# Optimization experiments

Hardware: AMD Instinct MI355X
Metric: run time of the kernel (lower is better)

Reference implementation:

```python
import jax, jax.numpy as jnp
import numpy as np

NFFT = 1024
HOP = 512
N_FREQ = NFFT // 2
B = 16
T = 4096


def _istft_kernels(nfft):
    # Same construction as _get_istft_kernels in the torch source.
    t = np.arange(nfft, dtype=np.float64)[:, None]
    f = np.arange(nfft // 2 + 1, dtype=np.float64)[None, :]
    k = np.exp(1j * (2.0 * np.pi * t * f) / nfft)  # [nfft, nfft/2+1]
    ac_cof = float(np.real(k[0, 0]))  # == 1.0
    k = 2.0 * k[:, 1:]
    k[:, -1] = k[:, -1] / 2.0
    return (np.real(k).astype(np.float32),  # [nfft, n_freq]
            np.imag(k).astype(np.float32),
            ac_cof)


def setup_inputs() -> dict:
    key = jax.random.key(0)
    k1, k2, k3 = jax.random.split(key, 3)
    magn = jax.random.normal(k1, (B, 1, N_FREQ, T), dtype=jnp.float32)
    phase = jax.random.normal(k2, (B, 1, N_FREQ, T), dtype=jnp.float32)
    ac = jax.random.normal(k3, (B, 1, T), dtype=jnp.float32)
    rk, ik, _ = _istft_kernels(NFFT)
    return {
        "magn": magn,
        "phase": phase,
        "ac": ac,
        "real_kernels": jnp.asarray(rk),   # [nfft, n_freq]
        "imag_kernels": jnp.asarray(ik),   # [nfft, n_freq]
    }


def reference(magn, phase, ac, real_kernels, imag_kernels):
    nfft, hop = NFFT, HOP
    ac_cof = 1.0  # real(exp(0)) from kernels[0, 0]
    real_part = jnp.einsum('bft,of->bot', magn[:, 0], real_kernels)   # [B, nfft, T]
    imag_part = jnp.einsum('bft,of->bot', -phase[:, 0], imag_kernels)  # [B, nfft, T]
    frames = (real_part - imag_part + ac_cof * ac) / float(nfft)       # ac [B,1,T] broadcasts
    # conv_transpose2d with identity kernel [nfft,1,1,nfft], stride=hop == overlap-add
    b, _, t = frames.shape
    out_len = (t - 1) * hop + nfft
    idx = jnp.arange(t)[:, None] * hop + jnp.arange(nfft)[None, :]     # [T, nfft]
    sig = jnp.zeros((b, out_len), frames.dtype)
    sig = sig.at[:, idx].add(jnp.swapaxes(frames, 1, 2))               # scatter-add frames
    return sig
```

## Files before the change

### kernel.cpp

```cpp
#include <hip/hip_runtime.h>
#include <hip/hip_bf16.h>

typedef __bf16 bf16;
typedef __bf16 bf16x4 __attribute__((ext_vector_type(4)));
typedef __bf16 bf16x8 __attribute__((ext_vector_type(8)));
typedef float  f32x4  __attribute__((ext_vector_type(4)));

#define T_SZ   4096
#define NFREQ  512
#define HOP    512
#define OUT_LEN 2097664
#define NTT33  33
#define XROWS  4097

#define XW_ELEMS ((size_t)16 * XROWS * 1024)
#define WT_ELEMS ((size_t)512 * 1024)
#define WS_NEED  ((XW_ELEMS + WT_ELEMS) * 2)

__device__ __forceinline__ void gl16(const void* g, void* l) {
    __builtin_amdgcn_global_load_lds(
        (const __attribute__((address_space(1))) void*)g,
        (__attribute__((address_space(3))) void*)l, 16, 0, 0);
}


__global__ __launch_bounds__(256, 4) void cvt_w(const float* __restrict__ rk,
                                                const float* __restrict__ ik,
                                                bf16* __restrict__ Wt) {
    const int j  = blockIdx.x;
    const int k4 = threadIdx.x * 4;
    const float* s = (k4 < NFREQ) ? &rk[j * NFREQ + k4] : &ik[j * NFREQ + k4 - NFREQ];
    f32x4 v = *(const f32x4*)s;
    bf16x4 h;
    h[0] = (bf16)v[0]; h[1] = (bf16)v[1]; h[2] = (bf16)v[2]; h[3] = (bf16)v[3];
    *(bf16x4*)&Wt[((size_t)j << 10) + k4] = h;
}

__global__ __launch_bounds__(256, 4) void cvt_x(const float* __restrict__ magn,
                                                const float* __restrict__ phase,
                                                bf16* __restrict__ Xw) {
    __shared__ float t2[64][133];
    const int tid = threadIdx.x;
    const int bid = blockIdx.x;
    const int kt  = bid & 15;
    const int tt  = (bid >> 4) & 31;
    const int b   = bid >> 9;
    const float* srcb = (kt < 8 ? magn : phase)
                      + ((size_t)b * NFREQ + (kt & 7) * 64) * T_SZ + tt * 128;
    const int fr = tid >> 5;
    const int cc = (tid & 31) * 4;
    #pragma unroll
    for (int p = 0; p < 8; ++p) {
        const int f = fr + 8 * p;
        f32x4 v = *(const f32x4*)&srcb[(size_t)f * T_SZ + cc];
        t2[f][cc + 0] = v[0]; t2[f][cc + 1] = v[1];
        t2[f][cc + 2] = v[2]; t2[f][cc + 3] = v[3];
    }
    if (tid < 64)
        t2[tid][128] = (tt > 0) ? srcb[(size_t)tid * T_SZ - 1] : 0.f;
    __syncthreads();

    const int koff = (tid & 7) * 8;
    bf16* dstb = Xw + (((size_t)b * XROWS + tt * 128) << 10) + kt * 64 + koff;
    #pragma unroll
    for (int q = 0; q < 4; ++q) {
        const int tr  = (tid >> 3) + 32 * q;
        const int im1 = tr ? (tr - 1) : 128;
        bf16x8 o;
        #pragma unroll
        for (int ki = 0; ki < 8; ++ki) {
            const int f = koff + ki;
            const float sgn = (f & 1) ? 1.f : -1.f;
            o[ki] = (bf16)(t2[f][tr] + sgn * t2[f][im1]);
        }
        *(bf16x8*)&dstb[(size_t)tr << 10] = o;
    }
    if (tt == 31 && tid < 8) {
        bf16x8 o;
        #pragma unroll
        for (int ki = 0; ki < 8; ++ki) {
            const int f = tid * 8 + ki;
            const float sgn = (f & 1) ? 1.f : -1.f;
            o[ki] = (bf16)(sgn * t2[f][127]);
        }
        *(bf16x8*)&Xw[(((size_t)b * XROWS + 4096) << 10) + kt * 64 + tid * 8] = o;
    }
}

__global__ __launch_bounds__(512, 4) void istft_gemmY(
    const bf16* __restrict__ Xw, const bf16* __restrict__ Wt,
    const float* __restrict__ acv, float* __restrict__ out)
{
    __shared__ __attribute__((aligned(16))) bf16 As[2][128 * 32];
    __shared__ __attribute__((aligned(16))) bf16 Bs[2][256 * 32];

    const int tid = threadIdx.x;
    const int w   = tid >> 6;
    const int l   = tid & 63;
    const int wr  = w >> 2, wc = w & 3;
    const int c15 = l & 15, c4 = l >> 4;

    const int bid = blockIdx.x;
    const int xcd = bid & 7;
    const int jt  = (bid >> 3) & 3;
    const int pg  = bid >> 5;
    const int pnl = pg * 8 + xcd;
    const int b   = pnl / 17;
    const int tt0 = pnl - b * 17;
    const int j0  = jt * 128;
    const int t0  = tt0 * 256;
    const size_t xb = (size_t)b * XROWS;

    const int ssrc = ((l & 3) ^ ((l >> 2) & 3) ^ ((l >> 4) & 3)) * 8;
    const int srow = 16 * w + (l >> 2);
    const size_t asrc = ((size_t)(j0 + srow)) << 10;
    int tq0 = t0 + srow;        if (tq0 > 4096) tq0 = 4096;
    int tq1 = t0 + 128 + srow;  if (tq1 > 4096) tq1 = 4096;
    const size_t bsrc0 = (xb + tq0) << 10;
    const size_t bsrc1 = (xb + tq1) << 10;

    auto stage = [&](int p, int ks) {
        const int k0 = ks * 32;
        gl16(Wt + asrc + k0 + ssrc, &As[p][(16 * w) * 32]);
        gl16(Xw + bsrc0 + k0 + ssrc, &Bs[p][(16 * w) * 32]);
        gl16(Xw + bsrc1 + k0 + ssrc, &Bs[p][(128 + 16 * w) * 32]);
    };

    f32x4 acc[4][4];
    #pragma unroll
    for (int i = 0; i < 4; ++i)
        #pragma unroll
        for (int j = 0; j < 4; ++j)
            acc[i][j] = (f32x4){0.f, 0.f, 0.f, 0.f};

    bf16x8 a[4], bb[4];
    auto rdFrags = [&](int p) {
        #pragma unroll
        for (int m = 0; m < 4; ++m) {
            const int r = wr * 64 + m * 16 + c15;
            const int s = ((c4 ^ r ^ (r >> 2)) & 3) * 8;
            a[m] = *(const bf16x8*)&As[p][r * 32 + s];
        }
        #pragma unroll
        for (int n = 0; n < 4; ++n) {
            const int r = wc * 64 + n * 16 + c15;
            const int s = ((c4 ^ r ^ (r >> 2)) & 3) * 8;
            bb[n] = *(const bf16x8*)&Bs[p][r * 32 + s];
        }
    };

    stage(0, 0);
    __syncthreads();

    for (int ks = 0; ks < 32; ++ks) {
        const int P = ks & 1;
        if (ks + 1 < 32) stage(P ^ 1, ks + 1);
        rdFrags(P);
        #pragma unroll
        for (int m = 0; m < 4; ++m)
            #pragma unroll
            for (int n = 0; n < 4; ++n)
                acc[m][n] = __builtin_amdgcn_mfma_f32_16x16x32_bf16(
                    a[m], bb[n], acc[m][n], 0, 0, 0);
        __syncthreads();
    }

    const float inv = 1.0f / 1024.0f;
    float* ob = out + (size_t)b * OUT_LEN;
    const float* acb = acv + (size_t)b * T_SZ;
    const int jbase = j0 + wr * 64 + c4 * 4;
    #pragma unroll
    for (int n = 0; n < 4; ++n) {
        const int tt = t0 + wc * 64 + n * 16 + c15;
        if (tt <= 4096) {
            const float acs = (tt < T_SZ ? acb[tt] : 0.f) + (tt ? acb[tt - 1] : 0.f);
            #pragma unroll
            for (int m = 0; m < 4; ++m) {
                f32x4 v;
                #pragma unroll
                for (int rr = 0; rr < 4; ++rr)
                    v[rr] = (acc[m][n][rr] + acs) * inv;
                __builtin_nontemporal_store(v, (f32x4*)&ob[(size_t)tt * HOP + jbase + m * 16]);
            }
        }
    }
}

#define LDBL 40
__global__ __launch_bounds__(256, 2) void istft_fused_legacy(
    const float* __restrict__ magn, const float* __restrict__ phase,
    const float* __restrict__ acv,
    const float* __restrict__ rk,  const float* __restrict__ ik,
    float* __restrict__ out)
{
    __shared__ __attribute__((aligned(16))) bf16 As[2][128 * LDBL];
    __shared__ __attribute__((aligned(16))) bf16 Bs[2][129 * LDBL];
    const int tid = threadIdx.x;
    const int w = tid >> 6, l = tid & 63;
    const int bid = blockIdx.x;
    const int xcd = bid & 7, q = bid >> 3;
    const int jt = q & 7, pgrp = q >> 3;
    const int pnl = pgrp * 8 + xcd;
    const int b = pnl / NTT33, tt0 = pnl - b * NTT33;
    const int j0 = jt * 64, t0 = tt0 * 128;
    const float* xm = magn  + (size_t)b * NFREQ * T_SZ;
    const float* xp = phase + (size_t)b * NFREQ * T_SZ;
    const int jrow = tid >> 3, fc = (tid & 7) * 4;
    const int f0 = (tid >> 5) * 4, tl = tid & 31;
    f32x4 areg[4]; float vreg[4][4]; float rz = 0.f;
    f32x4 acc[8][2];
    #pragma unroll
    for (int i = 0; i < 8; ++i)
        #pragma unroll
        for (int j = 0; j < 2; ++j) acc[i][j] = (f32x4){0.f, 0.f, 0.f, 0.f};
    const int nbase = w * 32;
    auto loadA = [&](int ks) {
        const int k0 = ks * 32;
        const float* wsrc = (k0 < NFREQ) ? (rk + k0) : (ik + (k0 - NFREQ));
        #pragma unroll
        for (int i = 0; i < 4; ++i) {
            const int jr = jrow + 32 * i;
            const int j = (jr < 64) ? (j0 + jr) : (j0 + 448 + jr);
            areg[i] = *(const f32x4*)&wsrc[(size_t)j * NFREQ + fc];
        }
    };
    auto writeA = [&](int p) {
        #pragma unroll
        for (int i = 0; i < 4; ++i) {
            bf16x4 v;
            v[0] = (bf16)areg[i][0]; v[1] = (bf16)areg[i][1];
            v[2] = (bf16)areg[i][2]; v[3] = (bf16)areg[i][3];
            *(bf16x4*)&As[p][(jrow + 32 * i) * LDBL + fc] = v;
        }
    };
    auto loadB = [&](int ks) {
        const int k0 = ks * 32;
        const float* xbp = (k0 < NFREQ) ? (xm + (size_t)k0 * T_SZ)
                                        : (xp + (size_t)(k0 - NFREQ) * T_SZ);
        #pragma unroll
        for (int i = 0; i < 4; ++i) {
            if (t0 + 32 * i + 32 <= T_SZ) {
                #pragma unroll
                for (int fj = 0; fj < 4; ++fj)
                    vreg[fj][i] = xbp[(size_t)(f0 + fj) * T_SZ + t0 + tl + 32 * i];
            } else {
                #pragma unroll
                for (int fj = 0; fj < 4; ++fj) vreg[fj][i] = 0.f;
            }
        }
        if (tid < 32) rz = (t0 >= 1) ? xbp[(size_t)tid * T_SZ + (t0 - 1)] : 0.f;
    };
    auto writeB = [&](int p) {
        #pragma unroll
        for (int i = 0; i < 4; ++i) {
            bf16x4 v;
            v[0] = (bf16)vreg[0][i]; v[1] = (bf16)vreg[1][i];
            v[2] = (bf16)vreg[2][i]; v[3] = (bf16)vreg[3][i];
            *(bf16x4*)&Bs[p][(1 + tl + 32 * i) * LDBL + f0] = v;
        }
        if (tid < 32) Bs[p][tid] = (bf16)rz;
    };
    loadA(0); loadB(0); writeA(0); writeB(0);
    __syncthreads();
    int p = 0;
    for (int ks = 0; ks < 32; ++ks) {
        if (ks + 1 < 32) { loadA(ks + 1); loadB(ks + 1); }
        bf16x8 af[8], blv[2], bhv[2];
        #pragma unroll
        for (int mi = 0; mi < 8; ++mi)
            af[mi] = *(const bf16x8*)&As[p][(mi * 16 + (l & 15)) * LDBL + (l >> 4) * 8];
        #pragma unroll
        for (int ni = 0; ni < 2; ++ni) {
            const int rb = nbase + ni * 16 + (l & 15);
            bhv[ni] = *(const bf16x8*)&Bs[p][rb * LDBL + (l >> 4) * 8];
            blv[ni] = *(const bf16x8*)&Bs[p][(rb + 1) * LDBL + (l >> 4) * 8];
        }
        #pragma unroll
        for (int ni = 0; ni < 2; ++ni)
            #pragma unroll
            for (int mi = 0; mi < 4; ++mi) {
                acc[mi][ni] = __builtin_amdgcn_mfma_f32_16x16x32_bf16(af[mi], blv[ni], acc[mi][ni], 0, 0, 0);
                acc[mi + 4][ni] = __builtin_amdgcn_mfma_f32_16x16x32_bf16(af[mi + 4], bhv[ni], acc[mi + 4][ni], 0, 0, 0);
            }
        if (ks + 1 < 32) { writeA(p ^ 1); writeB(p ^ 1); }
        __syncthreads();
        p ^= 1;
    }
    const float inv = 1.0f / 1024.0f;
    float* ob = out + (size_t)b * OUT_LEN;
    const float* acb = acv + (size_t)b * T_SZ;
    #pragma unroll
    for (int ni = 0; ni < 2; ++ni) {
        const int tt = t0 + nbase + ni * 16 + (l & 15);
        if (tt <= T_SZ) {
            float acs = 0.f;
            if (tt < T_SZ) acs += acb[tt];
            if (tt >= 1)   acs += acb[tt - 1];
            #pragma unroll
            for (int mi = 0; mi < 4; ++mi) {
                const int jl = j0 + mi * 16 + (l >> 4) * 4;
                f32x4 v;
                #pragma unroll
                for (int rr = 0; rr < 4; ++rr)
                    v[rr] = (acc[mi][ni][rr] + acc[mi + 4][ni][rr] + acs) * inv;
                __builtin_nontemporal_store(v, (f32x4*)&ob[(size_t)tt * HOP + jl]);
            }
        }
    }
}

extern "C" void kernel_launch(void* const* d_in, const int* in_sizes, int n_in,
                              void* d_out, int out_size, void* d_ws, size_t ws_size,
                              hipStream_t stream) {
    const float* magn  = (const float*)d_in[0];
    const float* phase = (const float*)d_in[1];
    const float* ac    = (const float*)d_in[2];
    const float* rk    = (const float*)d_in[3];
    const float* ik    = (const float*)d_in[4];
    float* out = (float*)d_out;

    if (ws_size >= WS_NEED) {
        bf16* Xw = (bf16*)d_ws;
        bf16* Wt = Xw + XW_ELEMS;
        cvt_w<<<512, 256, 0, stream>>>(rk, ik, Wt);
        cvt_x<<<8192, 256, 0, stream>>>(magn, phase, Xw);
        istft_gemmY<<<1088, 512, 0, stream>>>(Xw, Wt, ac, out);
    } else {
        istft_fused_legacy<<<528 * 8, 256, 0, stream>>>(magn, phase, ac, rk, ik, out);
    }
}
```

Measured before the change: 179.3 us.

## Split GEMM into even 128x128 tiles and move the ragged last row to a tail kernel

The main GEMM changes from 512-thread blocks with 128x256 tiles (17 t-tiles per batch, the last one ragged) to 256-thread blocks with 128x128 tiles over exactly 4096 rows, so the grid is uniform and the bounds checks go away. The single leftover output row (t=4096) is computed by a separate small GEMV kernel with 16 blocks. This is meant to remove load imbalance and tail waste from the padded tile. In exchange each tile reuses less data and the extra launch adds overhead.

After: 205.3 us. 14.5% more time.

```diff
diff --git a/kernel.cpp b/kernel.cpp
--- a/kernel.cpp
+++ b/kernel.cpp
@@ -87,17 +87,17 @@
     }
 }
 
-__global__ __launch_bounds__(512, 4) void istft_gemmY(
+__global__ __launch_bounds__(256, 4) void istft_gemmY2(
     const bf16* __restrict__ Xw, const bf16* __restrict__ Wt,
     const float* __restrict__ acv, float* __restrict__ out)
 {
     __shared__ __attribute__((aligned(16))) bf16 As[2][128 * 32];
-    __shared__ __attribute__((aligned(16))) bf16 Bs[2][256 * 32];
+    __shared__ __attribute__((aligned(16))) bf16 Bs[2][128 * 32];
 
     const int tid = threadIdx.x;
     const int w   = tid >> 6;
     const int l   = tid & 63;
-    const int wr  = w >> 2, wc = w & 3;
+    const int wr  = w >> 1, wc = w & 1;
     const int c15 = l & 15, c4 = l >> 4;
 
     const int bid = blockIdx.x;
@@ -105,25 +105,26 @@
     const int jt  = (bid >> 3) & 3;
     const int pg  = bid >> 5;
     const int pnl = pg * 8 + xcd;
-    const int b   = pnl / 17;
-    const int tt0 = pnl - b * 17;
+    const int b   = pnl >> 5;
+    const int tt0 = pnl & 31;
     const int j0  = jt * 128;
-    const int t0  = tt0 * 256;
+    const int t0  = tt0 * 128;
     const size_t xb = (size_t)b * XROWS;
 
     const int ssrc = ((l & 3) ^ ((l >> 2) & 3) ^ ((l >> 4) & 3)) * 8;
     const int srow = 16 * w + (l >> 2);
-    const size_t asrc = ((size_t)(j0 + srow)) << 10;
-    int tq0 = t0 + srow;        if (tq0 > 4096) tq0 = 4096;
-    int tq1 = t0 + 128 + srow;  if (tq1 > 4096) tq1 = 4096;
-    const size_t bsrc0 = (xb + tq0) << 10;
-    const size_t bsrc1 = (xb + tq1) << 10;
+
+    const size_t asrc0 = ((size_t)(j0 + srow)) << 10;
+    const size_t asrc1 = ((size_t)(j0 + 64 + srow)) << 10;
+    const size_t bsrc0 = (xb + t0 + srow) << 10;
+    const size_t bsrc1 = (xb + t0 + 64 + srow) << 10;
 
     auto stage = [&](int p, int ks) {
         const int k0 = ks * 32;
-        gl16(Wt + asrc + k0 + ssrc, &As[p][(16 * w) * 32]);
+        gl16(Wt + asrc0 + k0 + ssrc, &As[p][(16 * w) * 32]);
+        gl16(Wt + asrc1 + k0 + ssrc, &As[p][(64 + 16 * w) * 32]);
         gl16(Xw + bsrc0 + k0 + ssrc, &Bs[p][(16 * w) * 32]);
-        gl16(Xw + bsrc1 + k0 + ssrc, &Bs[p][(128 + 16 * w) * 32]);
+        gl16(Xw + bsrc1 + k0 + ssrc, &Bs[p][(64 + 16 * w) * 32]);
     };
 
     f32x4 acc[4][4];
@@ -172,18 +173,48 @@
     #pragma unroll
     for (int n = 0; n < 4; ++n) {
         const int tt = t0 + wc * 64 + n * 16 + c15;
-        if (tt <= 4096) {
-            const float acs = (tt < T_SZ ? acb[tt] : 0.f) + (tt ? acb[tt - 1] : 0.f);
+        const float acs = acb[tt] + (tt ? acb[tt - 1] : 0.f);
+        #pragma unroll
+        for (int m = 0; m < 4; ++m) {
+            f32x4 v;
             #pragma unroll
-            for (int m = 0; m < 4; ++m) {
-                f32x4 v;
-                #pragma unroll
-                for (int rr = 0; rr < 4; ++rr)
-                    v[rr] = (acc[m][n][rr] + acs) * inv;
-                __builtin_nontemporal_store(v, (f32x4*)&ob[(size_t)tt * HOP + jbase + m * 16]);
-            }
-        }
-    }
+            for (int rr = 0; rr < 4; ++rr)
+                v[rr] = (acc[m][n][rr] + acs) * inv;
+            __builtin_nontemporal_store(v, (f32x4*)&ob[(size_t)tt * HOP + jbase + m * 16]);
+        }
+    }
+}
+
+__global__ __launch_bounds__(256, 2) void istft_tailY(
+    const bf16* __restrict__ Xw, const bf16* __restrict__ Wt,
+    const float* __restrict__ acv, float* __restrict__ out)
+{
+    __shared__ float xf[1024];
+    const int b = blockIdx.x, tid = threadIdx.x;
+    const bf16* xr = Xw + (((size_t)b * XROWS + 4096) << 10);
+    {
+        bf16x4 v = *(const bf16x4*)&xr[tid * 4];
+        xf[tid * 4 + 0] = (float)v[0]; xf[tid * 4 + 1] = (float)v[1];
+        xf[tid * 4 + 2] = (float)v[2]; xf[tid * 4 + 3] = (float)v[3];
+    }
+    __syncthreads();
+    const float acs = acv[b * T_SZ + 4095];
+    float s0 = 0.f, s1 = 0.f;
+    const bf16* w0 = Wt + ((size_t)tid << 10);
+    const bf16* w1 = Wt + ((size_t)(tid + 256) << 10);
+    for (int kc = 0; kc < 128; ++kc) {
+        bf16x8 av = *(const bf16x8*)&w0[kc * 8];
+        bf16x8 cv = *(const bf16x8*)&w1[kc * 8];
+        #pragma unroll
+        for (int e = 0; e < 8; ++e) {
+            const float xv = xf[kc * 8 + e];
+            s0 += xv * (float)av[e];
+            s1 += xv * (float)cv[e];
+        }
+    }
+    float* ob = out + (size_t)b * OUT_LEN + (size_t)4096 * HOP;
+    ob[tid]       = (s0 + acs) * (1.f / 1024.f);
+    ob[tid + 256] = (s1 + acs) * (1.f / 1024.f);
 }
 
 #define LDBL 40
@@ -324,7 +355,8 @@
         bf16* Wt = Xw + XW_ELEMS;
         cvt_w<<<512, 256, 0, stream>>>(rk, ik, Wt);
         cvt_x<<<8192, 256, 0, stream>>>(magn, phase, Xw);
-        istft_gemmY<<<1088, 512, 0, stream>>>(Xw, Wt, ac, out);
+        istft_gemmY2<<<2048, 256, 0, stream>>>(Xw, Wt, ac, out);
+        istft_tailY<<<16, 256, 0, stream>>>(Xw, Wt, ac, out);
     } else {
         istft_fused_legacy<<<528 * 8, 256, 0, stream>>>(magn, phase, ac, rk, ik, out);
     }
```

## Use 128x128 GEMM tiles with triple-buffered LDS and one barrier per step

Applied to the files above, without the earlier changes.

Shrinks the GEMM block from 512 threads on a 128x256 tile to 256 threads on a 128x128 tile, which doubles the grid to 2112 blocks and remaps the XCD-aware tile indexing to 33 time tiles per batch. Replaces the double-buffered LDS with a three-stage ring, prefetching two k-steps ahead. Each step uses a partial vmcnt wait plus a raw s_barrier instead of __syncthreads, so loads overlap compute. The ac bias is hoisted into registers before the main loop. Smaller tiles lower arithmetic intensity and increase redundant operand loads, in exchange for deeper prefetch and more resident blocks.

New measurement: 181.7 us. Within noise of the previous version (+1.4%).

```diff
diff --git a/kernel.cpp b/kernel.cpp
--- a/kernel.cpp
+++ b/kernel.cpp
@@ -16,6 +16,8 @@
 #define XW_ELEMS ((size_t)16 * XROWS * 1024)
 #define WT_ELEMS ((size_t)512 * 1024)
 #define WS_NEED  ((XW_ELEMS + WT_ELEMS) * 2)
+
+#define SB()  __builtin_amdgcn_sched_barrier(0)
 
 __device__ __forceinline__ void gl16(const void* g, void* l) {
     __builtin_amdgcn_global_load_lds(
@@ -87,44 +89,58 @@
     }
 }
 
-__global__ __launch_bounds__(512, 4) void istft_gemmY(
+__global__ __launch_bounds__(256, 3) void istft_gemmY3(
     const bf16* __restrict__ Xw, const bf16* __restrict__ Wt,
     const float* __restrict__ acv, float* __restrict__ out)
 {
-    __shared__ __attribute__((aligned(16))) bf16 As[2][128 * 32];
-    __shared__ __attribute__((aligned(16))) bf16 Bs[2][256 * 32];
+    __shared__ __attribute__((aligned(16))) bf16 As[3][128 * 32];
+    __shared__ __attribute__((aligned(16))) bf16 Bs[3][128 * 32];
 
     const int tid = threadIdx.x;
     const int w   = tid >> 6;
     const int l   = tid & 63;
-    const int wr  = w >> 2, wc = w & 3;
+    const int wr  = w >> 1, wc = w & 1;
     const int c15 = l & 15, c4 = l >> 4;
 
     const int bid = blockIdx.x;
     const int xcd = bid & 7;
-    const int jt  = (bid >> 3) & 3;
-    const int pg  = bid >> 5;
-    const int pnl = pg * 8 + xcd;
-    const int b   = pnl / 17;
-    const int tt0 = pnl - b * 17;
+    const int idx = bid >> 3;
+    const int jt  = idx & 3;
+    const int png = idx >> 2;
+    const int pnl = png * 8 + xcd;
+    const int b   = pnl / NTT33;
+    const int tt0 = pnl - b * NTT33;
     const int j0  = jt * 128;
-    const int t0  = tt0 * 256;
+    const int t0  = tt0 * 128;
     const size_t xb = (size_t)b * XROWS;
 
     const int ssrc = ((l & 3) ^ ((l >> 2) & 3) ^ ((l >> 4) & 3)) * 8;
     const int srow = 16 * w + (l >> 2);
-    const size_t asrc = ((size_t)(j0 + srow)) << 10;
+
+    const size_t asrc0 = ((size_t)(j0 + srow)) << 10;
+    const size_t asrc1 = ((size_t)(j0 + 64 + srow)) << 10;
     int tq0 = t0 + srow;        if (tq0 > 4096) tq0 = 4096;
-    int tq1 = t0 + 128 + srow;  if (tq1 > 4096) tq1 = 4096;
+    int tq1 = t0 + 64 + srow;   if (tq1 > 4096) tq1 = 4096;
     const size_t bsrc0 = (xb + tq0) << 10;
     const size_t bsrc1 = (xb + tq1) << 10;
 
     auto stage = [&](int p, int ks) {
         const int k0 = ks * 32;
-        gl16(Wt + asrc + k0 + ssrc, &As[p][(16 * w) * 32]);
+        gl16(Wt + asrc0 + k0 + ssrc, &As[p][(16 * w) * 32]);
+        gl16(Wt + asrc1 + k0 + ssrc, &As[p][(64 + 16 * w) * 32]);
         gl16(Xw + bsrc0 + k0 + ssrc, &Bs[p][(16 * w) * 32]);
-        gl16(Xw + bsrc1 + k0 + ssrc, &Bs[p][(128 + 16 * w) * 32]);
-    };
+        gl16(Xw + bsrc1 + k0 + ssrc, &Bs[p][(64 + 16 * w) * 32]);
+    };
+
+    const float* acb = acv + (size_t)b * T_SZ;
+    float acs_r[4];
+    #pragma unroll
+    for (int n = 0; n < 4; ++n) {
+        const int tt = t0 + wc * 64 + n * 16 + c15;
+        const float a0 = (tt < T_SZ) ? acb[tt] : 0.f;
+        const float a1 = (tt >= 1 && tt <= T_SZ) ? acb[tt - 1] : 0.f;
+        acs_r[n] = a0 + a1;
+    }
 
     f32x4 acc[4][4];
     #pragma unroll
@@ -150,36 +166,40 @@
     };
 
     stage(0, 0);
-    __syncthreads();
-
+    stage(1, 1);
+    asm volatile("s_waitcnt vmcnt(4)" ::: "memory");
+    SB(); __builtin_amdgcn_s_barrier(); SB();
+
+    int cur = 0, nxt2 = 2;
     for (int ks = 0; ks < 32; ++ks) {
-        const int P = ks & 1;
-        if (ks + 1 < 32) stage(P ^ 1, ks + 1);
-        rdFrags(P);
+        if (ks + 2 < 32) stage(nxt2, ks + 2);
+        rdFrags(cur);
         #pragma unroll
         for (int m = 0; m < 4; ++m)
             #pragma unroll
             for (int n = 0; n < 4; ++n)
                 acc[m][n] = __builtin_amdgcn_mfma_f32_16x16x32_bf16(
                     a[m], bb[n], acc[m][n], 0, 0, 0);
-        __syncthreads();
+        if (ks < 30) asm volatile("s_waitcnt vmcnt(4)" ::: "memory");
+        else         asm volatile("s_waitcnt vmcnt(0)" ::: "memory");
+        SB(); __builtin_amdgcn_s_barrier(); SB();
+        cur  = (cur == 2)  ? 0 : cur + 1;
+        nxt2 = (nxt2 == 2) ? 0 : nxt2 + 1;
     }
 
     const float inv = 1.0f / 1024.0f;
     float* ob = out + (size_t)b * OUT_LEN;
-    const float* acb = acv + (size_t)b * T_SZ;
     const int jbase = j0 + wr * 64 + c4 * 4;
     #pragma unroll
     for (int n = 0; n < 4; ++n) {
         const int tt = t0 + wc * 64 + n * 16 + c15;
         if (tt <= 4096) {
-            const float acs = (tt < T_SZ ? acb[tt] : 0.f) + (tt ? acb[tt - 1] : 0.f);
             #pragma unroll
             for (int m = 0; m < 4; ++m) {
                 f32x4 v;
                 #pragma unroll
                 for (int rr = 0; rr < 4; ++rr)
-                    v[rr] = (acc[m][n][rr] + acs) * inv;
+                    v[rr] = (acc[m][n][rr] + acs_r[n]) * inv;
                 __builtin_nontemporal_store(v, (f32x4*)&ob[(size_t)tt * HOP + jbase + m * 16]);
             }
         }
@@ -324,7 +344,7 @@
         bf16* Wt = Xw + XW_ELEMS;
         cvt_w<<<512, 256, 0, stream>>>(rk, ik, Wt);
         cvt_x<<<8192, 256, 0, stream>>>(magn, phase, Xw);
-        istft_gemmY<<<1088, 512, 0, stream>>>(Xw, Wt, ac, out);
+        istft_gemmY3<<<2112, 256, 0, stream>>>(Xw, Wt, ac, out);
     } else {
         istft_fused_legacy<<<528 * 8, 256, 0, stream>>>(magn, phase, ac, rk, ik, out);
     }
```
